# Optimization experiments

Measured on AMD Instinct MI355X. Metric: run time of the kernel, lower is better.

Reference implementation:

```python
import jax, jax.numpy as jnp
import numpy as np

N = 50000          # nodes
E = 800000         # edges
IN = 256           # input feature dim
HID = 64           # hidden per-head dim
OUT = 64           # output dim
H1, H2 = 4, 1      # heads per layer
NEG_SLOPE = 0.2    # DGL GATConv default


def setup_inputs() -> dict:
    key = jax.random.key(0)
    ks = jax.random.split(key, 12)
    features = jax.random.normal(ks[0], (N, IN), dtype=jnp.float32)
    src = jax.random.randint(ks[1], (E,), 0, N, dtype=jnp.int32)
    dst = jax.random.randint(ks[2], (E,), 0, N, dtype=jnp.int32)
    s1 = 1.0 / np.sqrt(IN)
    s2 = 1.0 / np.sqrt(HID * H1)
    W1 = jax.random.normal(ks[3], (IN, H1 * HID), dtype=jnp.float32) * s1
    al1 = jax.random.normal(ks[4], (H1, HID), dtype=jnp.float32) * 0.1
    ar1 = jax.random.normal(ks[5], (H1, HID), dtype=jnp.float32) * 0.1
    b1 = jnp.zeros((H1, HID), dtype=jnp.float32)
    W2 = jax.random.normal(ks[6], (H1 * HID, H2 * OUT), dtype=jnp.float32) * s2
    al2 = jax.random.normal(ks[7], (H2, OUT), dtype=jnp.float32) * 0.1
    ar2 = jax.random.normal(ks[8], (H2, OUT), dtype=jnp.float32) * 0.1
    b2 = jnp.zeros((H2, OUT), dtype=jnp.float32)
    return {"features": features, "src": src, "dst": dst,
            "W1": W1, "al1": al1, "ar1": ar1, "b1": b1,
            "W2": W2, "al2": al2, "ar2": ar2, "b2": b2}


def gat_layer(h, src, dst, W, al, ar, b, heads, out_dim, activate):
    # projection: (N, H, D)
    feat = (h @ W).reshape(N, heads, out_dim)
    # per-node attention halves: (N, H)
    el = jnp.einsum('nhd,hd->nh', feat, al)
    er = jnp.einsum('nhd,hd->nh', feat, ar)
    # edge logits with leaky relu: (E, H)
    e = el[src] + er[dst]
    e = jnp.where(e >= 0, e, NEG_SLOPE * e)
    # edge softmax grouped by destination node
    emax = jax.ops.segment_max(e, dst, num_segments=N)      # (N, H)
    ee = jnp.exp(e - emax[dst])
    esum = jax.ops.segment_sum(ee, dst, num_segments=N)     # (N, H)
    alpha = ee / esum[dst]                                  # (E, H)
    # weighted scatter-sum of source features: (N, H, D)
    msg = alpha[:, :, None] * feat[src]
    out = jax.ops.segment_sum(msg, dst, num_segments=N) + b[None]
    if activate:
        out = jax.nn.relu(out)
    return out


def reference(features, src, dst, W1, al1, ar1, b1, W2, al2, ar2, b2):
    h = gat_layer(features, src, dst, W1, al1, ar1, b1, H1, HID, True)
    h = h.reshape(N, H1 * HID)                 # flatten(1)
    h = gat_layer(h, src, dst, W2, al2, ar2, b2, H2, OUT, False)
    return h.mean(axis=1)                      # mean over heads -> (N, OUT)
```

## Files before the change

### kernel.cpp

```cpp
#include <hip/hip_runtime.h>
#include <hip/hip_fp16.h>

#define NN   50000
#define NE   800000
#define IND  256
#define HIDD 64
#define OUTD 64
#define NH1  4
#define NH2  1
#define NEG  0.2f

#define NBUK 196
#define NCHK 256
#define CE   3125
#define MAXDEG 96

typedef float f32x4 __attribute__((ext_vector_type(4)));
typedef short s16x8 __attribute__((ext_vector_type(8)));

__device__ __forceinline__ short bf16_rne(float f) {
    unsigned u = __float_as_uint(f);
    unsigned r = u + 0x7FFFu + ((u >> 16) & 1u);
    return (short)(r >> 16);
}
__device__ __forceinline__ float bf16_tof(short h) {
    unsigned u = ((unsigned)(unsigned short)h) << 16;
    return __uint_as_float(u);
}
__device__ __forceinline__ void split_bf16(float f, short& hi, short& lo) {
    hi = bf16_rne(f);
    lo = bf16_rne(f - bf16_tof(hi));
}

__global__ void cnt1a_k(const int* __restrict__ key, int* __restrict__ cnt) {
    __shared__ int lc[NBUK];
    int tid = threadIdx.x, chunk = blockIdx.x;
    for (int j = tid; j < NBUK; j += 256) lc[j] = 0;
    __syncthreads();
    const int* kc = key + (size_t)chunk * CE;
    for (int t = tid; t < CE; t += 256) atomicAdd(&lc[kc[t] >> 8], 1);
    __syncthreads();
    for (int j = tid; j < NBUK; j += 256) cnt[j * NCHK + chunk] = lc[j];
}

__global__ void cnt1b_k(const int2* __restrict__ ein, int* __restrict__ cnt) {
    __shared__ int lc[NBUK];
    int tid = threadIdx.x, chunk = blockIdx.x;
    for (int j = tid; j < NBUK; j += 256) lc[j] = 0;
    __syncthreads();
    const int2* ec = ein + (size_t)chunk * CE;
    for (int t = tid; t < CE; t += 256) atomicAdd(&lc[ec[t].y >> 8], 1);
    __syncthreads();
    for (int j = tid; j < NBUK; j += 256) cnt[j * NCHK + chunk] = lc[j];
}

__global__ void scanC_k(int* __restrict__ cnt, int* __restrict__ buktot) {
    int b    = blockIdx.x * 4 + (threadIdx.x >> 6);
    int lane = threadIdx.x & 63;
    if (b >= NBUK) return;
    int base = b * NCHK + lane * 4;
    int4 v = *(int4*)&cnt[base];
    int s0 = v.x, s1 = s0 + v.y, s2 = s1 + v.z, s3 = s2 + v.w;
    int inc = s3;
    for (int o = 1; o < 64; o <<= 1) {
        int t = __shfl_up(inc, o);
        if (lane >= o) inc += t;
    }
    int excl = inc - s3;
    int4 w;
    w.x = excl; w.y = excl + s0; w.z = excl + s1; w.w = excl + s2;
    *(int4*)&cnt[base] = w;
    if (lane == 63) buktot[b] = inc;
}

__global__ void scanB_k(const int* __restrict__ buktot, int* __restrict__ bukbase) {
    __shared__ int tmp[256];
    int tid = threadIdx.x;
    int v = (tid < NBUK) ? buktot[tid] : 0;
    tmp[tid] = v;
    __syncthreads();
    for (int o = 1; o < 256; o <<= 1) {
        int add = (tid >= o) ? tmp[tid - o] : 0;
        __syncthreads();
        tmp[tid] += add;
        __syncthreads();
    }
    if (tid < NBUK) bukbase[tid] = tmp[tid] - v;
    if (tid == 0) bukbase[NBUK] = NE;
}

__global__ void fill1a_k(const int* __restrict__ src, const int* __restrict__ dst,
                         const int* __restrict__ cnt, const int* __restrict__ bukbase,
                         int2* __restrict__ eout) {
    __shared__ int cur[NBUK];
    int tid = threadIdx.x, chunk = blockIdx.x;
    for (int j = tid; j < NBUK; j += 256) cur[j] = cnt[j * NCHK + chunk] + bukbase[j];
    __syncthreads();
    size_t base = (size_t)chunk * CE;
    for (int t = tid; t < CE; t += 256) {
        int s = src[base + t], d = dst[base + t];
        int pos = atomicAdd(&cur[s >> 8], 1);
        eout[pos] = make_int2(s, d);
    }
}

__global__ void fill1b_k(const int2* __restrict__ ein, const int* __restrict__ cnt,
                         const int* __restrict__ bukbase, int2* __restrict__ eout) {
    __shared__ int cur[NBUK];
    int tid = threadIdx.x, chunk = blockIdx.x;
    for (int j = tid; j < NBUK; j += 256) cur[j] = cnt[j * NCHK + chunk] + bukbase[j];
    __syncthreads();
    const int2* ec = ein + (size_t)chunk * CE;
    for (int t = tid; t < CE; t += 256) {
        int2 e = ec[t];
        int pos = atomicAdd(&cur[e.y >> 8], 1);
        eout[pos] = e;
    }
}

__global__ void fill2_k(const int2* __restrict__ ein, const int* __restrict__ bukbase,
                        int* __restrict__ off, int* __restrict__ deg,
                        int* __restrict__ src_sorted) {
    __shared__ int lh[256];
    __shared__ int tmp[256];
    __shared__ int cur[256];
    int tid = threadIdx.x, b = blockIdx.x;
    int beg = bukbase[b], end = bukbase[b + 1];
    int node0 = b << 8;
    lh[tid] = 0;
    __syncthreads();
    for (int e = beg + tid; e < end; e += 256)
        atomicAdd(&lh[ein[e].y - node0], 1);
    __syncthreads();
    int v = lh[tid];
    tmp[tid] = v;
    __syncthreads();
    for (int o = 1; o < 256; o <<= 1) {
        int add = (tid >= o) ? tmp[tid - o] : 0;
        __syncthreads();
        tmp[tid] += add;
        __syncthreads();
    }
    int excl = tmp[tid] - v;
    int node = node0 + tid;
    if (node < NN) { deg[node] = v; off[node] = beg + excl; }
    cur[tid] = excl;
    __syncthreads();
    for (int e = beg + tid; e < end; e += 256) {
        int2 ed = ein[e];
        int r = atomicAdd(&cur[ed.y - node0], 1);
        src_sorted[beg + r] = ed.x;
    }
}

__global__ void wsplit2_k(const float* __restrict__ W1, const float* __restrict__ W2,
                          short* __restrict__ Wh1, short* __restrict__ Wl1,
                          short* __restrict__ Wh2, short* __restrict__ Wl2) {
    int idx = blockIdx.x * 256 + threadIdx.x;
    if (idx < IND * IND) {
        int k = idx / IND, n = idx - k * IND;
        short hi, lo;
        split_bf16(W1[idx], hi, lo);
        Wh1[(size_t)n * IND + k] = hi;
        Wl1[(size_t)n * IND + k] = lo;
    } else if (idx < IND * IND + IND * OUTD) {
        int i2 = idx - IND * IND;
        int k = i2 / OUTD, n = i2 - k * OUTD;
        short hi, lo;
        split_bf16(W2[i2], hi, lo);
        Wh2[(size_t)n * IND + k] = hi;
        Wl2[(size_t)n * IND + k] = lo;
    }
}

__global__ __launch_bounds__(256) void gemm_l1(const float* __restrict__ A,
                                               const short* __restrict__ Bt_hi,
                                               const short* __restrict__ Bt_lo,
                                               const float* __restrict__ al,
                                               const float* __restrict__ ar,
                                               __half* __restrict__ C,
                                               float* __restrict__ el,
                                               float* __restrict__ er, int M) {
    const int K = 256;
    __shared__ short As[64][40];
    __shared__ short Bs_hi[256][40];
    __shared__ short Bs_lo[256][40];

    int tid  = threadIdx.x;
    int wid  = tid >> 6, lane = tid & 63;
    int wm   = (wid >> 1) * 32;
    int wn   = (wid & 1) * 128;
    int row0 = blockIdx.x * 64;

    int arow = tid >> 2;
    int aseg = (tid & 3) * 8;
    int mr   = lane & 15;
    int kg   = (lane >> 4) * 8;

    f32x4 acc[2][8];
#pragma unroll
    for (int i = 0; i < 2; ++i)
#pragma unroll
        for (int j = 0; j < 8; ++j) acc[i][j] = (f32x4)(0.f);

    for (int k0 = 0; k0 < K; k0 += 32) {
        {
            int r = row0 + arow;
            float v[8];
            if (r < M) {
                float4 f0 = *(const float4*)&A[(size_t)r * K + k0 + aseg];
                float4 f1 = *(const float4*)&A[(size_t)r * K + k0 + aseg + 4];
                v[0] = f0.x; v[1] = f0.y; v[2] = f0.z; v[3] = f0.w;
                v[4] = f1.x; v[5] = f1.y; v[6] = f1.z; v[7] = f1.w;
            } else {
#pragma unroll
                for (int q = 0; q < 8; ++q) v[q] = 0.f;
            }
            short hi[8];
#pragma unroll
            for (int q = 0; q < 8; ++q) hi[q] = bf16_rne(v[q]);
            *(s16x8*)&As[arow][aseg] = *(s16x8*)&hi[0];
        }
        {
#pragma unroll
            for (int rep = 0; rep < 4; ++rep) {
                int n = rep * 64 + (tid >> 2);
                int ks = (tid & 3) * 8;
                *(s16x8*)&Bs_hi[n][ks] = *(const s16x8*)&Bt_hi[(size_t)n * K + k0 + ks];
                *(s16x8*)&Bs_lo[n][ks] = *(const s16x8*)&Bt_lo[(size_t)n * K + k0 + ks];
            }
        }
        __syncthreads();

        s16x8 ah[2];
#pragma unroll
        for (int mi = 0; mi < 2; ++mi)
            ah[mi] = *(const s16x8*)&As[wm + mi * 16 + mr][kg];
#pragma unroll
        for (int ni = 0; ni < 8; ++ni) {
            s16x8 bhv = *(const s16x8*)&Bs_hi[wn + ni * 16 + mr][kg];
            s16x8 blv = *(const s16x8*)&Bs_lo[wn + ni * 16 + mr][kg];
#pragma unroll
            for (int mi = 0; mi < 2; ++mi) {
                acc[mi][ni] = __builtin_amdgcn_mfma_f32_16x16x32_bf16(ah[mi], bhv, acc[mi][ni], 0, 0, 0);
                acc[mi][ni] = __builtin_amdgcn_mfma_f32_16x16x32_bf16(ah[mi], blv, acc[mi][ni], 0, 0, 0);
            }
        }
        __syncthreads();
    }

    float av[8], rv[8];
#pragma unroll
    for (int ni = 0; ni < 8; ++ni) {
        int c = wn + ni * 16 + mr;
        av[ni] = al[c];
        rv[ni] = ar[c];
    }
    int h0 = wn >> 6;

#pragma unroll
    for (int mi = 0; mi < 2; ++mi) {
#pragma unroll
        for (int r4 = 0; r4 < 4; ++r4) {
            int rr = row0 + wm + mi * 16 + (lane >> 4) * 4 + r4;
            if (rr < M) {
#pragma unroll
                for (int ni = 0; ni < 8; ++ni)
                    C[(size_t)rr * 256 + wn + ni * 16 + mr] = __float2half(acc[mi][ni][r4]);
            }
            float e0 = 0.f, e1 = 0.f, f0 = 0.f, f1 = 0.f;
#pragma unroll
            for (int ni = 0; ni < 4; ++ni) {
                e0 += acc[mi][ni][r4] * av[ni];
                f0 += acc[mi][ni][r4] * rv[ni];
            }
#pragma unroll
            for (int ni = 4; ni < 8; ++ni) {
                e1 += acc[mi][ni][r4] * av[ni];
                f1 += acc[mi][ni][r4] * rv[ni];
            }
#pragma unroll
            for (int o = 1; o <= 8; o <<= 1) {
                e0 += __shfl_xor(e0, o); e1 += __shfl_xor(e1, o);
                f0 += __shfl_xor(f0, o); f1 += __shfl_xor(f1, o);
            }
            if (mr == 0 && rr < M) {
                el[rr * 4 + h0]     = e0;
                el[rr * 4 + h0 + 1] = e1;
                er[rr * 4 + h0]     = f0;
                er[rr * 4 + h0 + 1] = f1;
            }
        }
    }
}

__global__ __launch_bounds__(256) void gemm_l2(const short* __restrict__ A,
                                               const short* __restrict__ Bt_hi,
                                               const short* __restrict__ Bt_lo,
                                               const float* __restrict__ al,
                                               const float* __restrict__ ar,
                                               __half* __restrict__ C,
                                               float* __restrict__ el,
                                               float* __restrict__ er, int M) {
    const int K = 256;
    __shared__ short As[128][40];
    __shared__ short Bs_hi[64][40];
    __shared__ short Bs_lo[64][40];

    int tid  = threadIdx.x;
    int wid  = tid >> 6, lane = tid & 63;
    int wm   = wid * 32;
    int row0 = blockIdx.x * 128;

    int arow = tid >> 1;
    int aseg = (tid & 1) * 16;
    int mr   = lane & 15;
    int kg   = (lane >> 4) * 8;

    f32x4 acc[2][4];
#pragma unroll
    for (int i = 0; i < 2; ++i)
#pragma unroll
        for (int j = 0; j < 4; ++j) acc[i][j] = (f32x4)(0.f);

    for (int k0 = 0; k0 < K; k0 += 32) {
        {
            int r = row0 + arow;
            if (r < M) {
                *(s16x8*)&As[arow][aseg]     = *(const s16x8*)&A[(size_t)r * K + k0 + aseg];
                *(s16x8*)&As[arow][aseg + 8] = *(const s16x8*)&A[(size_t)r * K + k0 + aseg + 8];
            } else {
                s16x8 z = (s16x8)(short)0;
                *(s16x8*)&As[arow][aseg]     = z;
                *(s16x8*)&As[arow][aseg + 8] = z;
            }
        }
        {
            int n  = tid >> 2;
            int ks = (tid & 3) * 8;
            *(s16x8*)&Bs_hi[n][ks] = *(const s16x8*)&Bt_hi[(size_t)n * K + k0 + ks];
            *(s16x8*)&Bs_lo[n][ks] = *(const s16x8*)&Bt_lo[(size_t)n * K + k0 + ks];
        }
        __syncthreads();

        s16x8 av_[2];
#pragma unroll
        for (int mi = 0; mi < 2; ++mi)
            av_[mi] = *(const s16x8*)&As[wm + mi * 16 + mr][kg];
#pragma unroll
        for (int ni = 0; ni < 4; ++ni) {
            s16x8 bhv = *(const s16x8*)&Bs_hi[ni * 16 + mr][kg];
            s16x8 blv = *(const s16x8*)&Bs_lo[ni * 16 + mr][kg];
#pragma unroll
            for (int mi = 0; mi < 2; ++mi) {
                acc[mi][ni] = __builtin_amdgcn_mfma_f32_16x16x32_bf16(av_[mi], bhv, acc[mi][ni], 0, 0, 0);
                acc[mi][ni] = __builtin_amdgcn_mfma_f32_16x16x32_bf16(av_[mi], blv, acc[mi][ni], 0, 0, 0);
            }
        }
        __syncthreads();
    }

    float av[4], rv[4];
#pragma unroll
    for (int ni = 0; ni < 4; ++ni) {
        int c = ni * 16 + mr;
        av[ni] = al[c];
        rv[ni] = ar[c];
    }

#pragma unroll
    for (int mi = 0; mi < 2; ++mi) {
#pragma unroll
        for (int r4 = 0; r4 < 4; ++r4) {
            int rr = row0 + wm + mi * 16 + (lane >> 4) * 4 + r4;
            if (rr < M) {
#pragma unroll
                for (int ni = 0; ni < 4; ++ni)
                    C[(size_t)rr * 64 + ni * 16 + mr] = __float2half(acc[mi][ni][r4]);
            }
            float e0 = 0.f, f0 = 0.f;
#pragma unroll
            for (int ni = 0; ni < 4; ++ni) {
                e0 += acc[mi][ni][r4] * av[ni];
                f0 += acc[mi][ni][r4] * rv[ni];
            }
#pragma unroll
            for (int o = 1; o <= 8; o <<= 1) {
                e0 += __shfl_xor(e0, o);
                f0 += __shfl_xor(f0, o);
            }
            if (mr == 0 && rr < M) { el[rr] = e0; er[rr] = f0; }
        }
    }
}

__global__ void agg_sm_l1(const __half* __restrict__ feat, const float* __restrict__ el,
                          const float* __restrict__ er, const int* __restrict__ src_sorted,
                          const int* __restrict__ off, const int* __restrict__ deg,
                          const float* __restrict__ bias, short* __restrict__ out) {
    __shared__ float alds[4][MAXDEG * 4];
    int w    = threadIdx.x >> 6;
    int wid  = blockIdx.x * 4 + w;
    int lane = threadIdx.x & 63;
    if (wid >= NN) return;
    int e   = lane >> 5;
    int c8  = (lane & 31) * 8;
    int h   = (lane & 31) >> 3;
    int k   = lane & 7;
    int sub = e * 8 + k;
    int beg = off[wid], dg = deg[wid];
    float erdh = er[(size_t)wid * 4 + h];

    float sum = 0.f;
    for (int p = sub; p < dg; p += 16) {
        int s = src_sorted[beg + p];
        float x = el[(size_t)s * 4 + h] + erdh;
        x = (x >= 0.f) ? x : NEG * x;
        float ex = __expf(x);
        if (p < MAXDEG) alds[w][p * 4 + h] = ex;
        sum += ex;
    }
    sum += __shfl_xor(sum, 1);
    sum += __shfl_xor(sum, 2);
    sum += __shfl_xor(sum, 4);
    sum += __shfl_xor(sum, 32);
    float inv = (dg > 0) ? 1.f / sum : 0.f;

    float acc[8] = {};
    int p = e;
    for (; p + 2 < dg; p += 4) {
        int s0 = src_sorted[beg + p];
        int s1 = src_sorted[beg + p + 2];
        float a0, a1;
        if (p < MAXDEG) a0 = alds[w][p * 4 + h];
        else {
            float x = el[(size_t)s0 * 4 + h] + erdh;
            x = (x >= 0.f) ? x : NEG * x;
            a0 = __expf(x);
        }
        if (p + 2 < MAXDEG) a1 = alds[w][(p + 2) * 4 + h];
        else {
            float x = el[(size_t)s1 * 4 + h] + erdh;
            x = (x >= 0.f) ? x : NEG * x;
            a1 = __expf(x);
        }
        float4 r0 = *(const float4*)&feat[(size_t)s0 * 256 + c8];
        float4 r1 = *(const float4*)&feat[(size_t)s1 * 256 + c8];
        __half2* h0 = (__half2*)&r0;
        __half2* h1 = (__half2*)&r1;
#pragma unroll
        for (int q = 0; q < 4; ++q) {
            float2 f0 = __half22float2(h0[q]);
            float2 f1 = __half22float2(h1[q]);
            acc[2 * q]     += a0 * f0.x + a1 * f1.x;
            acc[2 * q + 1] += a0 * f0.y + a1 * f1.y;
        }
    }
    for (; p < dg; p += 2) {
        int s = src_sorted[beg + p];
        float a;
        if (p < MAXDEG) a = alds[w][p * 4 + h];
        else {
            float x = el[(size_t)s * 4 + h] + erdh;
            x = (x >= 0.f) ? x : NEG * x;
            a = __expf(x);
        }
        float4 raw = *(const float4*)&feat[(size_t)s * 256 + c8];
        __half2* hh = (__half2*)&raw;
#pragma unroll
        for (int q = 0; q < 4; ++q) {
            float2 f = __half22float2(hh[q]);
            acc[2 * q]     += a * f.x;
            acc[2 * q + 1] += a * f.y;
        }
    }
#pragma unroll
    for (int q = 0; q < 8; ++q) acc[q] += __shfl_xor(acc[q], 32);
    if (e == 0) {
        short ob[8];
#pragma unroll
        for (int q = 0; q < 8; ++q) {
            float v = fmaxf(acc[q] * inv + bias[c8 + q], 0.f);
            ob[q] = bf16_rne(v);
        }
        *(s16x8*)&out[(size_t)wid * 256 + c8] = *(s16x8*)&ob[0];
    }
}

__global__ void agg_sm_l2(const __half* __restrict__ feat, const float* __restrict__ el,
                          const float* __restrict__ er, const int* __restrict__ src_sorted,
                          const int* __restrict__ off, const int* __restrict__ deg,
                          const float* __restrict__ bias, float* __restrict__ out) {
    __shared__ float alds[4][MAXDEG];
    int w    = threadIdx.x >> 6;
    int wid  = blockIdx.x * 4 + w;
    int lane = threadIdx.x & 63;
    if (wid >= NN) return;
    int e   = lane >> 3;
    int c8  = (lane & 7) * 8;
    int beg = off[wid], dg = deg[wid];
    float erd = er[wid];

    float sum = 0.f;
    for (int p = lane; p < dg; p += 64) {
        int s = src_sorted[beg + p];
        float x = el[s] + erd;
        x = (x >= 0.f) ? x : NEG * x;
        float ex = __expf(x);
        if (p < MAXDEG) alds[w][p] = ex;
        sum += ex;
    }
#pragma unroll
    for (int o = 1; o <= 32; o <<= 1) sum += __shfl_xor(sum, o);
    float inv = (dg > 0) ? 1.f / sum : 0.f;

    float acc[8] = {};
    for (int p = 0; p < dg; p += 8) {
        if (p + e < dg) {
            int s = src_sorted[beg + p + e];
            float a;
            if (p + e < MAXDEG) a = alds[w][p + e];
            else {
                float x = el[s] + erd;
                x = (x >= 0.f) ? x : NEG * x;
                a = __expf(x);
            }
            float4 raw = *(const float4*)&feat[(size_t)s * 64 + c8];
            __half2* hh = (__half2*)&raw;
#pragma unroll
            for (int q = 0; q < 4; ++q) {
                float2 f = __half22float2(hh[q]);
                acc[2 * q]     += a * f.x;
                acc[2 * q + 1] += a * f.y;
            }
        }
    }
#pragma unroll
    for (int o = 8; o <= 32; o <<= 1)
#pragma unroll
        for (int q = 0; q < 8; ++q) acc[q] += __shfl_xor(acc[q], o);
    if (e == 0) {
        float4 b0 = *(const float4*)&bias[c8];
        float4 b1 = *(const float4*)&bias[c8 + 4];
        float4 o0 = make_float4(acc[0] * inv + b0.x, acc[1] * inv + b0.y,
                                acc[2] * inv + b0.z, acc[3] * inv + b0.w);
        float4 o1 = make_float4(acc[4] * inv + b1.x, acc[5] * inv + b1.y,
                                acc[6] * inv + b1.z, acc[7] * inv + b1.w);
        *(float4*)&out[(size_t)wid * 64 + c8]     = o0;
        *(float4*)&out[(size_t)wid * 64 + c8 + 4] = o1;
    }
}

extern "C" void kernel_launch(void* const* d_in, const int* in_sizes, int n_in,
                              void* d_out, int out_size, void* d_ws, size_t ws_size,
                              hipStream_t stream) {
    const float* features = (const float*)d_in[0];
    const int*   src      = (const int*)  d_in[1];
    const int*   dst      = (const int*)  d_in[2];
    const float* W1       = (const float*)d_in[3];
    const float* al1      = (const float*)d_in[4];
    const float* ar1      = (const float*)d_in[5];
    const float* b1       = (const float*)d_in[6];
    const float* W2       = (const float*)d_in[7];
    const float* al2      = (const float*)d_in[8];
    const float* ar2      = (const float*)d_in[9];
    const float* b2       = (const float*)d_in[10];
    float* out = (float*)d_out;

    char* base = (char*)d_ws;
    size_t o = 0;
    __half* feat1h = (__half*)(base + o); o += (size_t)NN * 256 * 2;
    short*  h1b    = (short*) (base + o); o += (size_t)NN * 256 * 2;
    float*  el1 = (float*)(base + o); o += (size_t)NN * 4 * 4;
    float*  er1 = (float*)(base + o); o += (size_t)NN * 4 * 4;
    float*  el2 = (float*)(base + o); o += (size_t)NN * 4;
    float*  er2 = (float*)(base + o); o += (size_t)NN * 4;
    int* deg        = (int*)(base + o); o += (size_t)NN * 4;
    int* off        = (int*)(base + o); o += (size_t)NN * 4;
    int* src_sorted = (int*)(base + o); o += (size_t)NE * 4;
    int* cnt        = (int*)(base + o); o += (size_t)NBUK * NCHK * 4;
    int* buktot     = (int*)(base + o); o += 1024;
    int* bukbase    = (int*)(base + o); o += 1024;
    int2* ebufS = (int2*)(base + o); o += (size_t)NE * 8;
    int2* ebufD = (int2*)(base + o); o += (size_t)NE * 8;
    short* Wt1_hi = (short*)(base + o); o += (size_t)IND * IND * 2;
    short* Wt1_lo = (short*)(base + o); o += (size_t)IND * IND * 2;
    short* Wt2_hi = (short*)(base + o); o += (size_t)OUTD * IND * 2;
    short* Wt2_lo = (short*)(base + o); o += (size_t)OUTD * IND * 2;

    __half* feat2h = feat1h;

    cnt1a_k<<<NCHK, 256, 0, stream>>>(src, cnt);
    scanC_k<<<(NBUK + 3) / 4, 256, 0, stream>>>(cnt, buktot);
    scanB_k<<<1, 256, 0, stream>>>(buktot, bukbase);
    fill1a_k<<<NCHK, 256, 0, stream>>>(src, dst, cnt, bukbase, ebufS);
    cnt1b_k<<<NCHK, 256, 0, stream>>>(ebufS, cnt);
    scanC_k<<<(NBUK + 3) / 4, 256, 0, stream>>>(cnt, buktot);
    scanB_k<<<1, 256, 0, stream>>>(buktot, bukbase);
    fill1b_k<<<NCHK, 256, 0, stream>>>(ebufS, cnt, bukbase, ebufD);
    fill2_k<<<NBUK, 256, 0, stream>>>(ebufD, bukbase, off, deg, src_sorted);

    wsplit2_k<<<(IND * IND + IND * OUTD + 255) / 256, 256, 0, stream>>>(
        W1, W2, Wt1_hi, Wt1_lo, Wt2_hi, Wt2_lo);

    gemm_l1<<<(NN + 63) / 64, 256, 0, stream>>>(features, Wt1_hi, Wt1_lo, al1, ar1,
                                                feat1h, el1, er1, NN);
    agg_sm_l1<<<(NN + 3) / 4, 256, 0, stream>>>(feat1h, el1, er1, src_sorted, off, deg,
                                                b1, h1b);

    gemm_l2<<<(NN + 127) / 128, 256, 0, stream>>>(h1b, Wt2_hi, Wt2_lo, al2, ar2,
                                                  feat2h, el2, er2, NN);
    agg_sm_l2<<<(NN + 3) / 4, 256, 0, stream>>>(feat2h, el2, er2, src_sorted, off, deg,
                                                b2, out);
}
```

Baseline: 195.9 us.

## Drop bf16 hi/lo weight split in GEMMs and fold bucket scan into fill kernels

The weights are now converted to a single bf16 copy instead of a hi+lo pair, which halves the MFMA count and the weight staging in shared memory for both projection GEMMs. The single-block bucket-base scan kernel is also removed: each fill kernel recomputes the 196-entry prefix sum in shared memory, saving two kernel launches. The trade-off is lower precision in the weight operand, with some risk to accuracy, plus redundant scan work in every block.

```diff
diff --git a/kernel.cpp b/kernel.cpp
--- a/kernel.cpp
+++ b/kernel.cpp
@@ -22,14 +22,6 @@
     unsigned u = __float_as_uint(f);
     unsigned r = u + 0x7FFFu + ((u >> 16) & 1u);
     return (short)(r >> 16);
-}
-__device__ __forceinline__ float bf16_tof(short h) {
-    unsigned u = ((unsigned)(unsigned short)h) << 16;
-    return __uint_as_float(u);
-}
-__device__ __forceinline__ void split_bf16(float f, short& hi, short& lo) {
-    hi = bf16_rne(f);
-    lo = bf16_rne(f - bf16_tof(hi));
 }
 
 __global__ void cnt1a_k(const int* __restrict__ key, int* __restrict__ cnt) {
@@ -73,9 +65,12 @@
     if (lane == 63) buktot[b] = inc;
 }
 
-__global__ void scanB_k(const int* __restrict__ buktot, int* __restrict__ bukbase) {
+__global__ void fill1a_k(const int* __restrict__ src, const int* __restrict__ dst,
+                         const int* __restrict__ cnt, const int* __restrict__ buktot,
+                         int2* __restrict__ eout) {
+    __shared__ int cur[NBUK];
     __shared__ int tmp[256];
-    int tid = threadIdx.x;
+    int tid = threadIdx.x, chunk = blockIdx.x;
     int v = (tid < NBUK) ? buktot[tid] : 0;
     tmp[tid] = v;
     __syncthreads();
@@ -85,16 +80,7 @@
         tmp[tid] += add;
         __syncthreads();
     }
-    if (tid < NBUK) bukbase[tid] = tmp[tid] - v;
-    if (tid == 0) bukbase[NBUK] = NE;
-}
-
-__global__ void fill1a_k(const int* __restrict__ src, const int* __restrict__ dst,
-                         const int* __restrict__ cnt, const int* __restrict__ bukbase,
-                         int2* __restrict__ eout) {
-    __shared__ int cur[NBUK];
-    int tid = threadIdx.x, chunk = blockIdx.x;
-    for (int j = tid; j < NBUK; j += 256) cur[j] = cnt[j * NCHK + chunk] + bukbase[j];
+    if (tid < NBUK) cur[tid] = cnt[tid * NCHK + chunk] + tmp[tid] - v;
     __syncthreads();
     size_t base = (size_t)chunk * CE;
     for (int t = tid; t < CE; t += 256) {
@@ -105,10 +91,20 @@
 }
 
 __global__ void fill1b_k(const int2* __restrict__ ein, const int* __restrict__ cnt,
-                         const int* __restrict__ bukbase, int2* __restrict__ eout) {
+                         const int* __restrict__ buktot, int2* __restrict__ eout) {
     __shared__ int cur[NBUK];
+    __shared__ int tmp[256];
     int tid = threadIdx.x, chunk = blockIdx.x;
-    for (int j = tid; j < NBUK; j += 256) cur[j] = cnt[j * NCHK + chunk] + bukbase[j];
+    int v = (tid < NBUK) ? buktot[tid] : 0;
+    tmp[tid] = v;
+    __syncthreads();
+    for (int o = 1; o < 256; o <<= 1) {
+        int add = (tid >= o) ? tmp[tid - o] : 0;
+        __syncthreads();
+        tmp[tid] += add;
+        __syncthreads();
+    }
+    if (tid < NBUK) cur[tid] = cnt[tid * NCHK + chunk] + tmp[tid] - v;
     __syncthreads();
     const int2* ec = ein + (size_t)chunk * CE;
     for (int t = tid; t < CE; t += 256) {
@@ -118,14 +114,25 @@
     }
 }
 
-__global__ void fill2_k(const int2* __restrict__ ein, const int* __restrict__ bukbase,
+__global__ void fill2_k(const int2* __restrict__ ein, const int* __restrict__ buktot,
                         int* __restrict__ off, int* __restrict__ deg,
                         int* __restrict__ src_sorted) {
     __shared__ int lh[256];
     __shared__ int tmp[256];
     __shared__ int cur[256];
     int tid = threadIdx.x, b = blockIdx.x;
-    int beg = bukbase[b], end = bukbase[b + 1];
+    int v0 = (tid < NBUK) ? buktot[tid] : 0;
+    tmp[tid] = v0;
+    __syncthreads();
+    for (int o = 1; o < 256; o <<= 1) {
+        int add = (tid >= o) ? tmp[tid - o] : 0;
+        __syncthreads();
+        tmp[tid] += add;
+        __syncthreads();
+    }
+    int beg = (b > 0) ? tmp[b - 1] : 0;
+    int end = tmp[b];
+    __syncthreads();
     int node0 = b << 8;
     lh[tid] = 0;
     __syncthreads();
@@ -153,29 +160,21 @@
     }
 }
 
-__global__ void wsplit2_k(const float* __restrict__ W1, const float* __restrict__ W2,
-                          short* __restrict__ Wh1, short* __restrict__ Wl1,
-                          short* __restrict__ Wh2, short* __restrict__ Wl2) {
+__global__ void wsplitT_k(const float* __restrict__ W1, const float* __restrict__ W2,
+                          short* __restrict__ Wh1, short* __restrict__ Wh2) {
     int idx = blockIdx.x * 256 + threadIdx.x;
     if (idx < IND * IND) {
         int k = idx / IND, n = idx - k * IND;
-        short hi, lo;
-        split_bf16(W1[idx], hi, lo);
-        Wh1[(size_t)n * IND + k] = hi;
-        Wl1[(size_t)n * IND + k] = lo;
+        Wh1[(size_t)n * IND + k] = bf16_rne(W1[idx]);
     } else if (idx < IND * IND + IND * OUTD) {
         int i2 = idx - IND * IND;
         int k = i2 / OUTD, n = i2 - k * OUTD;
-        short hi, lo;
-        split_bf16(W2[i2], hi, lo);
-        Wh2[(size_t)n * IND + k] = hi;
-        Wl2[(size_t)n * IND + k] = lo;
+        Wh2[(size_t)n * IND + k] = bf16_rne(W2[i2]);
     }
 }
 
 __global__ __launch_bounds__(256) void gemm_l1(const float* __restrict__ A,
-                                               const short* __restrict__ Bt_hi,
-                                               const short* __restrict__ Bt_lo,
+                                               const short* __restrict__ Bt,
                                                const float* __restrict__ al,
                                                const float* __restrict__ ar,
                                                __half* __restrict__ C,
@@ -183,8 +182,7 @@
                                                float* __restrict__ er, int M) {
     const int K = 256;
     __shared__ short As[64][40];
-    __shared__ short Bs_hi[256][40];
-    __shared__ short Bs_lo[256][40];
+    __shared__ short Bs[256][40];
 
     int tid  = threadIdx.x;
     int wid  = tid >> 6, lane = tid & 63;
@@ -226,8 +224,7 @@
             for (int rep = 0; rep < 4; ++rep) {
                 int n = rep * 64 + (tid >> 2);
                 int ks = (tid & 3) * 8;
-                *(s16x8*)&Bs_hi[n][ks] = *(const s16x8*)&Bt_hi[(size_t)n * K + k0 + ks];
-                *(s16x8*)&Bs_lo[n][ks] = *(const s16x8*)&Bt_lo[(size_t)n * K + k0 + ks];
+                *(s16x8*)&Bs[n][ks] = *(const s16x8*)&Bt[(size_t)n * K + k0 + ks];
             }
         }
         __syncthreads();
@@ -238,13 +235,10 @@
             ah[mi] = *(const s16x8*)&As[wm + mi * 16 + mr][kg];
 #pragma unroll
         for (int ni = 0; ni < 8; ++ni) {
-            s16x8 bhv = *(const s16x8*)&Bs_hi[wn + ni * 16 + mr][kg];
-            s16x8 blv = *(const s16x8*)&Bs_lo[wn + ni * 16 + mr][kg];
-#pragma unroll
-            for (int mi = 0; mi < 2; ++mi) {
+            s16x8 bhv = *(const s16x8*)&Bs[wn + ni * 16 + mr][kg];
+#pragma unroll
+            for (int mi = 0; mi < 2; ++mi)
                 acc[mi][ni] = __builtin_amdgcn_mfma_f32_16x16x32_bf16(ah[mi], bhv, acc[mi][ni], 0, 0, 0);
-                acc[mi][ni] = __builtin_amdgcn_mfma_f32_16x16x32_bf16(ah[mi], blv, acc[mi][ni], 0, 0, 0);
-            }
         }
         __syncthreads();
     }
@@ -295,8 +289,7 @@
 }
 
 __global__ __launch_bounds__(256) void gemm_l2(const short* __restrict__ A,
-                                               const short* __restrict__ Bt_hi,
-                                               const short* __restrict__ Bt_lo,
+                                               const short* __restrict__ Bt,
                                                const float* __restrict__ al,
                                                const float* __restrict__ ar,
                                                __half* __restrict__ C,
@@ -304,8 +297,7 @@
                                                float* __restrict__ er, int M) {
     const int K = 256;
     __shared__ short As[128][40];
-    __shared__ short Bs_hi[64][40];
-    __shared__ short Bs_lo[64][40];
+    __shared__ short Bs[64][40];
 
     int tid  = threadIdx.x;
     int wid  = tid >> 6, lane = tid & 63;
@@ -338,8 +330,7 @@
         {
             int n  = tid >> 2;
             int ks = (tid & 3) * 8;
-            *(s16x8*)&Bs_hi[n][ks] = *(const s16x8*)&Bt_hi[(size_t)n * K + k0 + ks];
-            *(s16x8*)&Bs_lo[n][ks] = *(const s16x8*)&Bt_lo[(size_t)n * K + k0 + ks];
+            *(s16x8*)&Bs[n][ks] = *(const s16x8*)&Bt[(size_t)n * K + k0 + ks];
         }
         __syncthreads();
 
@@ -349,13 +340,10 @@
             av_[mi] = *(const s16x8*)&As[wm + mi * 16 + mr][kg];
 #pragma unroll
         for (int ni = 0; ni < 4; ++ni) {
-            s16x8 bhv = *(const s16x8*)&Bs_hi[ni * 16 + mr][kg];
-            s16x8 blv = *(const s16x8*)&Bs_lo[ni * 16 + mr][kg];
-#pragma unroll
-            for (int mi = 0; mi < 2; ++mi) {
+            s16x8 bhv = *(const s16x8*)&Bs[ni * 16 + mr][kg];
+#pragma unroll
+            for (int mi = 0; mi < 2; ++mi)
                 acc[mi][ni] = __builtin_amdgcn_mfma_f32_16x16x32_bf16(av_[mi], bhv, acc[mi][ni], 0, 0, 0);
-                acc[mi][ni] = __builtin_amdgcn_mfma_f32_16x16x32_bf16(av_[mi], blv, acc[mi][ni], 0, 0, 0);
-            }
         }
         __syncthreads();
     }
@@ -580,35 +568,29 @@
     int* src_sorted = (int*)(base + o); o += (size_t)NE * 4;
     int* cnt        = (int*)(base + o); o += (size_t)NBUK * NCHK * 4;
     int* buktot     = (int*)(base + o); o += 1024;
-    int* bukbase    = (int*)(base + o); o += 1024;
     int2* ebufS = (int2*)(base + o); o += (size_t)NE * 8;
     int2* ebufD = (int2*)(base + o); o += (size_t)NE * 8;
-    short* Wt1_hi = (short*)(base + o); o += (size_t)IND * IND * 2;
-    short* Wt1_lo = (short*)(base + o); o += (size_t)IND * IND * 2;
-    short* Wt2_hi = (short*)(base + o); o += (size_t)OUTD * IND * 2;
-    short* Wt2_lo = (short*)(base + o); o += (size_t)OUTD * IND * 2;
+    short* Wt1 = (short*)(base + o); o += (size_t)IND * IND * 2;
+    short* Wt2 = (short*)(base + o); o += (size_t)OUTD * IND * 2;
 
     __half* feat2h = feat1h;
 
     cnt1a_k<<<NCHK, 256, 0, stream>>>(src, cnt);
     scanC_k<<<(NBUK + 3) / 4, 256, 0, stream>>>(cnt, buktot);
-    scanB_k<<<1, 256, 0, stream>>>(buktot, bukbase);
-    fill1a_k<<<NCHK, 256, 0, stream>>>(src, dst, cnt, bukbase, ebufS);
+    fill1a_k<<<NCHK, 256, 0, stream>>>(src, dst, cnt, buktot, ebufS);
     cnt1b_k<<<NCHK, 256, 0, stream>>>(ebufS, cnt);
     scanC_k<<<(NBUK + 3) / 4, 256, 0, stream>>>(cnt, buktot);
-    scanB_k<<<1, 256, 0, stream>>>(buktot, bukbase);
-    fill1b_k<<<NCHK, 256, 0, stream>>>(ebufS, cnt, bukbase, ebufD);
-    fill2_k<<<NBUK, 256, 0, stream>>>(ebufD, bukbase, off, deg, src_sorted);
-
-    wsplit2_k<<<(IND * IND + IND * OUTD + 255) / 256, 256, 0, stream>>>(
-        W1, W2, Wt1_hi, Wt1_lo, Wt2_hi, Wt2_lo);
-
-    gemm_l1<<<(NN + 63) / 64, 256, 0, stream>>>(features, Wt1_hi, Wt1_lo, al1, ar1,
+    fill1b_k<<<NCHK, 256, 0, stream>>>(ebufS, cnt, buktot, ebufD);
+    fill2_k<<<NBUK, 256, 0, stream>>>(ebufD, buktot, off, deg, src_sorted);
+
+    wsplitT_k<<<(IND * IND + IND * OUTD + 255) / 256, 256, 0, stream>>>(W1, W2, Wt1, Wt2);
+
+    gemm_l1<<<(NN + 63) / 64, 256, 0, stream>>>(features, Wt1, al1, ar1,
                                                 feat1h, el1, er1, NN);
     agg_sm_l1<<<(NN + 3) / 4, 256, 0, stream>>>(feat1h, el1, er1, src_sorted, off, deg,
                                                 b1, h1b);
 
-    gemm_l2<<<(NN + 127) / 128, 256, 0, stream>>>(h1b, Wt2_hi, Wt2_lo, al2, ar2,
+    gemm_l2<<<(NN + 127) / 128, 256, 0, stream>>>(h1b, Wt2, al2, ar2,
                                                   feat2h, el2, er2, NN);
     agg_sm_l2<<<(NN + 3) / 4, 256, 0, stream>>>(feat2h, el2, er2, src_sorted, off, deg,
                                                 b2, out);
```

After: 185.3 us. 5.4% less time.
